# Kernel tuning notes

Hardware: AMD Instinct MI355X
Metric: run time of the kernel (lower is better)

Reference implementation:

```python
import jax, jax.numpy as jnp
import numpy as np

D_MODEL = 1024


def setup_inputs() -> dict:
    key = jax.random.key(0)
    k_x, k_qkv, k_proj, k_b = jax.random.split(key, 4)
    b, t, d = 4, 2048, D_MODEL
    scale = 1.0 / np.sqrt(d)
    x = jax.random.normal(k_x, (b, t, d), dtype=jnp.float32)
    # torch Linear(d, 3d, bias=False): weight [3d, d]; we store transposed [d, 3d]
    w_qkv = jax.random.normal(k_qkv, (d, 3 * d), dtype=jnp.float32) * scale
    w_proj = jax.random.normal(k_proj, (d, d), dtype=jnp.float32) * scale
    b_proj = jax.random.normal(k_b, (d,), dtype=jnp.float32) * scale
    return {"x": x, "w_qkv": w_qkv, "w_proj": w_proj, "b_proj": b_proj}


def reference(x, w_qkv, w_proj, b_proj):
    b, t, d = x.shape
    qkv = jnp.einsum("btd,de->bte", x, w_qkv)  # [b, t, 3d]
    q, k, v = jnp.split(qkv, 3, axis=-1)
    att = jnp.einsum("btd,bsd->bts", q, k) / jnp.sqrt(jnp.float32(d))  # [b, t, t]
    causal = jnp.tril(jnp.ones((t, t), dtype=bool))
    att = jnp.where(causal, att, -jnp.inf)
    att = jax.nn.softmax(att, axis=-1)
    out = jnp.einsum("bts,bsd->btd", att, v)
    return jnp.einsum("btd,de->bte", out, w_proj) + b_proj
```

## Files before the change

kernel.cpp:

```cpp
#include <hip/hip_runtime.h>


typedef __bf16 bf16x8_t __attribute__((ext_vector_type(8)));
typedef float  f32x4_t  __attribute__((ext_vector_type(4)));
typedef unsigned short u16;

struct alignas(8) u16x4 { u16 x, y, z, w; };

__device__ inline float bf2f(u16 u) {
  union { unsigned u; float f; } c; c.u = ((unsigned)u) << 16; return c.f;
}
__device__ inline u16 f2bf(float f) {
  union { float f; unsigned u; } c; c.f = f;
  unsigned r = c.u + 0x7fffu + ((c.u >> 16) & 1u);
  return (u16)(r >> 16);
}

template<int OUTMODE, int GRIDMODE>
__global__ __launch_bounds__(256, 4)
void gemm_bt(const u16* __restrict__ A, const u16* __restrict__ B,
             void* __restrict__ Cv, u16* __restrict__ C2,
             const float* __restrict__ bias,
             int K, int lda, int ldb, int ldc,
             long sA, long sB, long sC)
{
  int bn0, bm0;
  if (GRIDMODE == 1) {
    const int x = blockIdx.x;
    int r = (int)((sqrtf(8.f * x + 1.f) - 1.f) * 0.5f);
    while ((r + 1) * (r + 2) / 2 <= x) ++r;
    while (r * (r + 1) / 2 > x) --r;
    bm0 = r * 128;
    bn0 = (x - r * (r + 1) / 2) * 128;
  } else if (GRIDMODE == 2) {
    bn0 = blockIdx.x * 128;
    bm0 = ((int)gridDim.y - 1 - (int)blockIdx.y) * 128;
  } else {
    bn0 = blockIdx.x * 128;
    bm0 = blockIdx.y * 128;
  }
  const long bz = blockIdx.z;
  const u16* Ab = A + bz * sA;
  const u16* Bb = B + bz * sB;
  const int Keff = (GRIDMODE == 2) ? min(K, bm0 + 128) : K;

  __shared__ __align__(16) u16 lA[2 * 128 * 32];
  __shared__ __align__(16) u16 lB[2 * 128 * 32];

  const int tid  = threadIdx.x;
  const int lane = tid & 63;
  const int wv   = tid >> 6;
  const int wm   = (wv >> 1) << 6;
  const int wn   = (wv & 1) << 6;
  const int l15  = lane & 15;
  const int rd_off = l15 * 64 + ((((lane >> 4) ^ (l15 >> 1)) & 3) << 4);

  f32x4_t acc[4][4];
#pragma unroll
  for (int i = 0; i < 4; ++i)
#pragma unroll
    for (int j = 0; j < 4; ++j)
      acc[i][j] = (f32x4_t){0.f, 0.f, 0.f, 0.f};

  float rsacc = 0.f;

  const long ldA2 = (long)lda * 2, ldB2 = (long)ldb * 2;
  const int c_src = (tid & 3) ^ ((tid >> 3) & 3);
  const char* pA = (const char*)(Ab + (long)bm0 * lda) + (long)(tid >> 2) * ldA2 + (c_src << 4);
  const char* pB = (const char*)(Bb + (long)bn0 * ldb) + (long)(tid >> 2) * ldB2 + (c_src << 4);
  const int ldsbo = tid * 16;

  for (int k0 = 0; k0 < Keff; k0 += 64) {
    const long kb = (long)k0 * 2;
#pragma unroll
    for (int r = 0; r < 4; ++r) {
      const long go = (long)(r & 1) * 64 * ldA2 + (r >> 1) * 64;
      __builtin_amdgcn_global_load_lds(
          (const __attribute__((address_space(1))) unsigned int*)(pA + kb + go),
          (__attribute__((address_space(3))) unsigned int*)((char*)lA + ldsbo + r * 4096), 16, 0, 0);
    }
#pragma unroll
    for (int r = 0; r < 4; ++r) {
      const long go = (long)(r & 1) * 64 * ldB2 + (r >> 1) * 64;
      __builtin_amdgcn_global_load_lds(
          (const __attribute__((address_space(1))) unsigned int*)(pB + kb + go),
          (__attribute__((address_space(3))) unsigned int*)((char*)lB + ldsbo + r * 4096), 16, 0, 0);
    }
    __syncthreads();

    const char* lAb = (const char*)lA + wm * 64 + rd_off;
    const char* lBb = (const char*)lB + wn * 64 + rd_off;
#pragma unroll
    for (int s = 0; s < 2; ++s) {
      const int so = s * 8192;
      bf16x8_t b0 = *(const bf16x8_t*)(lBb + so + 0 * 1024);
      bf16x8_t b1 = *(const bf16x8_t*)(lBb + so + 1 * 1024);
      bf16x8_t b2 = *(const bf16x8_t*)(lBb + so + 2 * 1024);
      bf16x8_t b3 = *(const bf16x8_t*)(lBb + so + 3 * 1024);
#pragma unroll
      for (int mf = 0; mf < 4; ++mf) {
        bf16x8_t a = *(const bf16x8_t*)(lAb + so + mf * 1024);
        acc[mf][0] = __builtin_amdgcn_mfma_f32_16x16x32_bf16(a, b0, acc[mf][0], 0, 0, 0);
        acc[mf][1] = __builtin_amdgcn_mfma_f32_16x16x32_bf16(a, b1, acc[mf][1], 0, 0, 0);
        acc[mf][2] = __builtin_amdgcn_mfma_f32_16x16x32_bf16(a, b2, acc[mf][2], 0, 0, 0);
        acc[mf][3] = __builtin_amdgcn_mfma_f32_16x16x32_bf16(a, b3, acc[mf][3], 0, 0, 0);
      }
    }

    if (OUTMODE == 4) {
      const int rr = tid >> 1;
      const int bsel = (tid & 1) * 8192;
#pragma unroll
      for (int c = 0; c < 4; ++c) {
        const int cc = (c + (rr >> 1)) & 3;
        bf16x8_t v = *(const bf16x8_t*)((const char*)lA + bsel + rr * 64 + cc * 16);
#pragma unroll
        for (int e = 0; e < 8; ++e) rsacc += (float)v[e];
      }
    }
    __syncthreads();
  }

  const int r4 = (lane >> 4) << 2;

  if (OUTMODE == 2) {
    if (bn0 >= 2048) {
#pragma unroll
      for (int mf = 0; mf < 4; ++mf) {
        const int s0 = bm0 + wm + mf * 16 + r4;
        const int b_ = s0 >> 11;
        const int s_ = s0 & 2047;
#pragma unroll
        for (int nf = 0; nf < 4; ++nf) {
          const int dcol = bn0 - 2048 + wn + nf * 16 + l15;
          u16x4 o = {f2bf(acc[mf][nf][0]), f2bf(acc[mf][nf][1]),
                     f2bf(acc[mf][nf][2]), f2bf(acc[mf][nf][3])};
          *(u16x4*)&C2[(((long)b_ * 1024 + dcol) << 11) + s_] = o;
        }
      }
    } else {
      u16* Cb16 = (u16*)Cv;
#pragma unroll
      for (int mf = 0; mf < 4; ++mf)
#pragma unroll
        for (int nf = 0; nf < 4; ++nf) {
          const int col = bn0 + wn + nf * 16 + l15;
#pragma unroll
          for (int r = 0; r < 4; ++r)
            Cb16[(long)(bm0 + wm + mf * 16 + r4 + r) * ldc + col] = f2bf(acc[mf][nf][r]);
        }
    }
    return;
  }

  if (OUTMODE == 3) {
    const float scale = 0.03125f;
    const bool diag = (bm0 == bn0);
    u16* Cb16 = (u16*)Cv + bz * sC;
#pragma unroll
    for (int mf = 0; mf < 4; ++mf)
#pragma unroll
      for (int r = 0; r < 4; ++r) {
        const int grow = bm0 + wm + mf * 16 + r4 + r;
#pragma unroll
        for (int nf = 0; nf < 4; ++nf) {
          const int col = bn0 + wn + nf * 16 + l15;
          float e = (diag && col > grow) ? 0.f : __expf(acc[mf][nf][r] * scale);
          Cb16[(long)grow * ldc + col] = f2bf(e);
        }
      }
    return;
  }

  if (OUTMODE == 4) {
    float* rsl = (float*)lA;
    rsl[tid] = rsacc;
    __syncthreads();
    float* rinv = (float*)lB;
    if (tid < 128) rinv[tid] = 1.0f / (rsl[2 * tid] + rsl[2 * tid + 1]);
    __syncthreads();
    u16* Cb16 = (u16*)Cv + bz * sC;
#pragma unroll
    for (int mf = 0; mf < 4; ++mf)
#pragma unroll
      for (int nf = 0; nf < 4; ++nf) {
        const int col = bn0 + wn + nf * 16 + l15;
#pragma unroll
        for (int r = 0; r < 4; ++r) {
          const int rl = wm + mf * 16 + r4 + r;
          Cb16[(long)(bm0 + rl) * ldc + col] = f2bf(acc[mf][nf][r] * rinv[rl]);
        }
      }
    return;
  }

  float* Cf32 = (float*)Cv + bz * sC;
#pragma unroll
  for (int mf = 0; mf < 4; ++mf)
#pragma unroll
    for (int nf = 0; nf < 4; ++nf) {
      const int col = bn0 + wn + nf * 16 + l15;
      const float bb = bias[col];
#pragma unroll
      for (int r = 0; r < 4; ++r)
        Cf32[(long)(bm0 + wm + mf * 16 + r4 + r) * ldc + col] = acc[mf][nf][r] + bb;
    }
}

__global__ __launch_bounds__(256)
void prep(const float* __restrict__ x, u16* __restrict__ xbf,
          const float* __restrict__ wqkv, u16* __restrict__ wqkvT,
          const float* __restrict__ wproj, u16* __restrict__ wprojT) {
  const int bid = blockIdx.x;
  if (bid < 8192) {
    const int i = bid * 256 + threadIdx.x;
    float4 v = ((const float4*)x)[i];
    u16x4 o = {f2bf(v.x), f2bf(v.y), f2bf(v.z), f2bf(v.w)};
    ((u16x4*)xbf)[i] = o;
    return;
  }
  const int tb = bid - 8192;
  const int bx = tb & 127;
  const int by = tb >> 7;
  const bool isq = bx < 96;
  const float* in = isq ? wqkv : wproj;
  u16* out        = isq ? wqkvT : wprojT;
  const int C     = isq ? 3072 : 1024;
  const int c0 = (isq ? bx : (bx - 96)) * 32;
  const int r0 = by * 32;
  __shared__ float t[32][33];
  const int tx = threadIdx.x & 31, ty = threadIdx.x >> 5;
#pragma unroll
  for (int i = 0; i < 32; i += 8)
    t[ty + i][tx] = in[(long)(r0 + ty + i) * C + (c0 + tx)];
  __syncthreads();
#pragma unroll
  for (int i = 0; i < 32; i += 8)
    out[(long)(c0 + ty + i) * 1024 + (r0 + tx)] = f2bf(t[tx][ty + i]);
}

extern "C" void kernel_launch(void* const* d_in, const int* in_sizes, int n_in,
                              void* d_out, int out_size, void* d_ws, size_t ws_size,
                              hipStream_t stream) {
  (void)in_sizes; (void)n_in; (void)out_size; (void)ws_size;
  const float* x      = (const float*)d_in[0];
  const float* w_qkv  = (const float*)d_in[1];
  const float* w_proj = (const float*)d_in[2];
  const float* b_proj = (const float*)d_in[3];
  float* y = (float*)d_out;
  char*  ws = (char*)d_ws;

  u16* xbf    = (u16*)(ws);
  u16* qk     = (u16*)(ws + (16l << 20));
  u16* wqkvT  = (u16*)(ws + (48l << 20));
  u16* wprojT = (u16*)(ws + (54l << 20));
  u16* vT     = (u16*)(ws + (56l << 20));
  u16* E      = (u16*)(ws + (72l << 20));
  u16* attn   = xbf;

  prep<<<12288, 256, 0, stream>>>(x, xbf, w_qkv, wqkvT, w_proj, wprojT);
  gemm_bt<2, 0><<<dim3(24, 64, 1), 256, 0, stream>>>(
      xbf, wqkvT, qk, vT, nullptr, 1024, 1024, 1024, 2048, 0, 0, 0);
  gemm_bt<3, 1><<<dim3(136, 1, 4), 256, 0, stream>>>(
      qk, qk + 1024, E, nullptr, nullptr, 1024, 2048, 2048, 2048,
      (long)2048 * 2048, (long)2048 * 2048, (long)2048 * 2048);
  gemm_bt<4, 2><<<dim3(8, 16, 4), 256, 0, stream>>>(
      E, vT, attn, nullptr, nullptr, 2048, 2048, 2048, 1024,
      (long)2048 * 2048, (long)1024 * 2048, (long)2048 * 1024);
  gemm_bt<1, 0><<<dim3(8, 64, 1), 256, 0, stream>>>(
      attn, wprojT, y, nullptr, b_proj, 1024, 1024, 1024, 1024, 0, 0, 0);
}
```

Before: 261.3 us.

## Split-K the causal PV GEMM with atomic fp32 accumulation and finalize pass

Replaces the triangular PV GEMM grid, where row blocks had very uneven K lengths, with a balanced split-K grid. Each row block's causal K range is divided into chunks of roughly four 128-wide tiles, and partial products are accumulated into an fp32 buffer with atomicAdd. Row sums are also accumulated atomically, only by the bn0==0 blocks. A new finalize kernel then normalizes the result and converts it to bf16. The change adds two memsets, a 32MB fp32 atomic buffer and an extra pass, in exchange for better load balance across the GPU.

After: 311.6 us. 19.2% more time.

```diff
diff --git a/kernel.cpp b/kernel.cpp
--- a/kernel.cpp
+++ b/kernel.cpp
@@ -20,11 +20,11 @@
 __global__ __launch_bounds__(256, 4)
 void gemm_bt(const u16* __restrict__ A, const u16* __restrict__ B,
              void* __restrict__ Cv, u16* __restrict__ C2,
-             const float* __restrict__ bias,
+             const float* __restrict__ bias, float* __restrict__ rs,
              int K, int lda, int ldb, int ldc,
              long sA, long sB, long sC)
 {
-  int bn0, bm0;
+  int bn0, bm0, kb0 = 0, kend = K;
   if (GRIDMODE == 1) {
     const int x = blockIdx.x;
     int r = (int)((sqrtf(8.f * x + 1.f) - 1.f) * 0.5f);
@@ -32,9 +32,23 @@
     while (r * (r + 1) / 2 > x) --r;
     bm0 = r * 128;
     bn0 = (x - r * (r + 1) / 2) * 128;
-  } else if (GRIDMODE == 2) {
-    bn0 = blockIdx.x * 128;
-    bm0 = ((int)gridDim.y - 1 - (int)blockIdx.y) * 128;
+  } else if (GRIDMODE == 3) {
+    const int xr = 39 - (int)blockIdx.x;
+    int rb = 0, cum = 0, nck = 1;
+    while (true) {
+      nck = (rb + 4) >> 2;
+      if (xr < cum + nck) break;
+      cum += nck; ++rb;
+    }
+    const int kc  = xr - cum;
+    const int tot = rb + 1;
+    const int q   = tot / nck, rem = tot % nck;
+    const int u0  = kc * q + min(kc, rem);
+    const int len = q + (kc < rem ? 1 : 0);
+    bm0 = rb * 128;
+    bn0 = blockIdx.y * 128;
+    kb0 = u0 * 128;
+    kend = (u0 + len) * 128;
   } else {
     bn0 = blockIdx.x * 128;
     bm0 = blockIdx.y * 128;
@@ -42,7 +56,6 @@
   const long bz = blockIdx.z;
   const u16* Ab = A + bz * sA;
   const u16* Bb = B + bz * sB;
-  const int Keff = (GRIDMODE == 2) ? min(K, bm0 + 128) : K;
 
   __shared__ __align__(16) u16 lA[2 * 128 * 32];
   __shared__ __align__(16) u16 lB[2 * 128 * 32];
@@ -70,7 +83,7 @@
   const char* pB = (const char*)(Bb + (long)bn0 * ldb) + (long)(tid >> 2) * ldB2 + (c_src << 4);
   const int ldsbo = tid * 16;
 
-  for (int k0 = 0; k0 < Keff; k0 += 64) {
+  for (int k0 = kb0; k0 < kend; k0 += 64) {
     const long kb = (long)k0 * 2;
 #pragma unroll
     for (int r = 0; r < 4; ++r) {
@@ -107,7 +120,7 @@
       }
     }
 
-    if (OUTMODE == 4) {
+    if (OUTMODE == 4 && bn0 == 0) {
       const int rr = tid >> 1;
       const int bsel = (tid & 1) * 8192;
 #pragma unroll
@@ -173,24 +186,23 @@
   }
 
   if (OUTMODE == 4) {
-    float* rsl = (float*)lA;
-    rsl[tid] = rsacc;
-    __syncthreads();
-    float* rinv = (float*)lB;
-    if (tid < 128) rinv[tid] = 1.0f / (rsl[2 * tid] + rsl[2 * tid + 1]);
-    __syncthreads();
-    u16* Cb16 = (u16*)Cv + bz * sC;
+    float* Cf32 = (float*)Cv + bz * sC;
 #pragma unroll
     for (int mf = 0; mf < 4; ++mf)
 #pragma unroll
       for (int nf = 0; nf < 4; ++nf) {
         const int col = bn0 + wn + nf * 16 + l15;
 #pragma unroll
-        for (int r = 0; r < 4; ++r) {
-          const int rl = wm + mf * 16 + r4 + r;
-          Cb16[(long)(bm0 + rl) * ldc + col] = f2bf(acc[mf][nf][r] * rinv[rl]);
-        }
-      }
+        for (int r = 0; r < 4; ++r)
+          atomicAdd(&Cf32[(long)(bm0 + wm + mf * 16 + r4 + r) * ldc + col],
+                    acc[mf][nf][r]);
+      }
+    if (bn0 == 0) {
+      float* rsl = (float*)lA;
+      rsl[tid] = rsacc;
+      __syncthreads();
+      if (tid < 128) atomicAdd(&rs[bz * 2048 + bm0 + tid], rsl[2 * tid] + rsl[2 * tid + 1]);
+    }
     return;
   }
 
@@ -239,6 +251,16 @@
     out[(long)(c0 + ty + i) * 1024 + (r0 + tx)] = f2bf(t[tx][ty + i]);
 }
 
+__global__ __launch_bounds__(256)
+void finalize_pv(const float* __restrict__ u, const float* __restrict__ rs,
+                 u16* __restrict__ o) {
+  const int i = blockIdx.x * 256 + threadIdx.x;
+  float4 v = ((const float4*)u)[i];
+  const float rinv = 1.0f / rs[i >> 8];
+  u16x4 t = {f2bf(v.x * rinv), f2bf(v.y * rinv), f2bf(v.z * rinv), f2bf(v.w * rinv)};
+  ((u16x4*)o)[i] = t;
+}
+
 extern "C" void kernel_launch(void* const* d_in, const int* in_sizes, int n_in,
                               void* d_out, int out_size, void* d_ws, size_t ws_size,
                               hipStream_t stream) {
@@ -256,17 +278,22 @@
   u16* wprojT = (u16*)(ws + (54l << 20));
   u16* vT     = (u16*)(ws + (56l << 20));
   u16* E      = (u16*)(ws + (72l << 20));
+  float* attnU = (float*)qk;
+  float* rsum  = (float*)wqkvT;
   u16* attn   = xbf;
 
   prep<<<12288, 256, 0, stream>>>(x, xbf, w_qkv, wqkvT, w_proj, wprojT);
   gemm_bt<2, 0><<<dim3(24, 64, 1), 256, 0, stream>>>(
-      xbf, wqkvT, qk, vT, nullptr, 1024, 1024, 1024, 2048, 0, 0, 0);
+      xbf, wqkvT, qk, vT, nullptr, nullptr, 1024, 1024, 1024, 2048, 0, 0, 0);
   gemm_bt<3, 1><<<dim3(136, 1, 4), 256, 0, stream>>>(
-      qk, qk + 1024, E, nullptr, nullptr, 1024, 2048, 2048, 2048,
+      qk, qk + 1024, E, nullptr, nullptr, nullptr, 1024, 2048, 2048, 2048,
       (long)2048 * 2048, (long)2048 * 2048, (long)2048 * 2048);
-  gemm_bt<4, 2><<<dim3(8, 16, 4), 256, 0, stream>>>(
-      E, vT, attn, nullptr, nullptr, 2048, 2048, 2048, 1024,
+  hipMemsetAsync(attnU, 0, (long)4 * 2048 * 1024 * sizeof(float), stream);
+  hipMemsetAsync(rsum, 0, 4 * 2048 * sizeof(float), stream);
+  gemm_bt<4, 3><<<dim3(40, 8, 4), 256, 0, stream>>>(
+      E, vT, attnU, nullptr, nullptr, rsum, 2048, 2048, 2048, 1024,
       (long)2048 * 2048, (long)1024 * 2048, (long)2048 * 1024);
+  finalize_pv<<<8192, 256, 0, stream>>>(attnU, rsum, attn);
   gemm_bt<1, 0><<<dim3(8, 64, 1), 256, 0, stream>>>(
-      attn, wprojT, y, nullptr, b_proj, 1024, 1024, 1024, 1024, 0, 0, 0);
-}
+      attn, wprojT, y, nullptr, b_proj, nullptr, 1024, 1024, 1024, 1024, 0, 0, 0);
+}
```
